# Kernel tuning notes

Measured on AMD Instinct MI355X. Metric: run time of the kernel, lower is better.

Reference implementation:

```python
import jax, jax.numpy as jnp
import numpy as np

N = 50000      # number of atoms/nodes
D = 32         # atom_dim == units (pad_length = 0)
E = 300000     # number of bonds/edges
BD = 16        # bond_dim
STEPS = 4      # message passing steps


def setup_inputs() -> dict:
    key = jax.random.key(0)
    ks = jax.random.split(key, 8)
    atom_features = jax.random.normal(ks[0], (N, D), dtype=jnp.float32)
    bond_features = jax.random.uniform(ks[1], (E, BD), dtype=jnp.float32)
    pair_indices = jax.random.randint(ks[2], (E, 2), 0, N, dtype=jnp.int32)
    # EdgeNetwork kernel: xavier_uniform on [bond_dim, atom_dim*atom_dim]
    s = float(np.sqrt(6.0 / (BD + D * D)))
    kernel = jax.random.uniform(ks[3], (BD, D * D), dtype=jnp.float32, minval=-s, maxval=s)
    bias = jnp.zeros((D * D,), dtype=jnp.float32)
    # torch.nn.GRUCell init: U(-1/sqrt(H), 1/sqrt(H)), H = D (pad_length = 0)
    stdv = float(1.0 / np.sqrt(D))
    W_ih = jax.random.uniform(ks[4], (3 * D, D), dtype=jnp.float32, minval=-stdv, maxval=stdv)
    W_hh = jax.random.uniform(ks[5], (3 * D, D), dtype=jnp.float32, minval=-stdv, maxval=stdv)
    b_ih = jax.random.uniform(ks[6], (3 * D,), dtype=jnp.float32, minval=-stdv, maxval=stdv)
    b_hh = jax.random.uniform(ks[7], (3 * D,), dtype=jnp.float32, minval=-stdv, maxval=stdv)
    return {
        "atom_features": atom_features,
        "bond_features": bond_features,
        "pair_indices": pair_indices,
        "kernel": kernel,
        "bias": bias,
        "W_ih": W_ih,
        "W_hh": W_hh,
        "b_ih": b_ih,
        "b_hh": b_hh,
    }


def _gru_cell(x, h, W_ih, W_hh, b_ih, b_hh):
    # torch.nn.GRUCell math, gates stacked as (r, z, n)
    gi = x @ W_ih.T + b_ih  # [N, 3D]
    gh = h @ W_hh.T + b_hh  # [N, 3D]
    i_r, i_z, i_n = jnp.split(gi, 3, axis=-1)
    h_r, h_z, h_n = jnp.split(gh, 3, axis=-1)
    r = jax.nn.sigmoid(i_r + h_r)
    z = jax.nn.sigmoid(i_z + h_z)
    n = jnp.tanh(i_n + r * h_n)
    return (1.0 - z) * n + z * h


def reference(atom_features, bond_features, pair_indices, kernel, bias, W_ih, W_hh, b_ih, b_hh):
    # pad_length = units - atom_dim = 0, so no padding needed.
    W = kernel.reshape(BD, D, D)   # per-bond-feature DxD transforms
    Bm = bias.reshape(D, D)        # bias as DxD matrix applied to neighbor feats
    dst = pair_indices[:, 0]       # aggregation (index_add) target
    src = pair_indices[:, 1]       # gathered neighbor

    h = atom_features
    for _ in range(STEPS):
        nbr = h[src]  # [E, D] gather
        # transformed[e, i] = sum_j (bond[e] @ kernel + bias)[i, j] * nbr[e, j]
        msg = jnp.einsum('eb,bij,ej->ei', bond_features, W, nbr) + nbr @ Bm.T
        agg = jax.ops.segment_sum(msg, dst, num_segments=N)  # scatter-add
        h = _gru_cell(agg, h, W_ih, W_hh, b_ih, b_hh)
    return h
```

## Files before the change

kernel.cpp:

```cpp
#include <hip/hip_runtime.h>
#include <math.h>

#define N_ATOMS 50000
#define D 32
#define E_EDGES 300000
#define BD 16
#define SW 544
#define PADN 50176
#define SCAN_BLOCKS 196
#define GRU_TILE 8
#define GRU_NT (N_ATOMS / GRU_TILE)

#define NB 16
#define FBLOCKS ((N_ATOMS + NB - 1) / NB)

__device__ __forceinline__ float sigmoidf_(float x) {
    return 1.0f / (1.0f + __expf(-x));
}


__global__ void k_build_wt(const float* __restrict__ kern,
                           const float* __restrict__ bias,
                           float* __restrict__ WTj) {
    int idx = blockIdx.x * 256 + threadIdx.x;
    if (idx >= 32 * SW) return;
    int j = idx / SW;
    int r = idx - j * SW;
    int b = r >> 5, i = r & 31;
    WTj[idx] = (b < BD) ? kern[b * 1024 + i * 32 + j] : bias[i * 32 + j];
}

__global__ void k_hist(const int* __restrict__ pair, int* __restrict__ deg) {
    int e = blockIdx.x * 256 + threadIdx.x;
    if (e < E_EDGES) atomicAdd(&deg[pair[2 * e + 1]], 1);
}

__global__ void k_scan1(const int* __restrict__ deg, int* __restrict__ offs,
                        int* __restrict__ bsums) {
    __shared__ int sm[256];
    int t = threadIdx.x, gid = blockIdx.x * 256 + t;
    int v = deg[gid];
    sm[t] = v;
    __syncthreads();
    for (int off = 1; off < 256; off <<= 1) {
        int x = (t >= off) ? sm[t - off] : 0;
        __syncthreads();
        sm[t] += x;
        __syncthreads();
    }
    offs[gid] = sm[t] - v;
    if (t == 255) bsums[blockIdx.x] = sm[255];
}

__global__ void k_scan2(const int* __restrict__ bsums, int* __restrict__ boffs, int nb) {
    __shared__ int sm[256];
    int t = threadIdx.x;
    int v = (t < nb) ? bsums[t] : 0;
    sm[t] = v;
    __syncthreads();
    for (int off = 1; off < 256; off <<= 1) {
        int x = (t >= off) ? sm[t - off] : 0;
        __syncthreads();
        sm[t] += x;
        __syncthreads();
    }
    if (t < nb) boffs[t] = sm[t] - v;
}

__global__ void k_scan3(int* __restrict__ offs, const int* __restrict__ boffs) {
    int gid = blockIdx.x * 256 + threadIdx.x;
    offs[gid] += boffs[blockIdx.x];
}

__global__ void k_scatter_perm(const int* __restrict__ pair, const int* __restrict__ offs,
                               int* __restrict__ cursor, const float* __restrict__ bond,
                               float* __restrict__ bond_perm, int* __restrict__ dstid) {
    int e = blockIdx.x * 256 + threadIdx.x;
    if (e >= E_EDGES) return;
    int d = pair[2 * e], s = pair[2 * e + 1];
    int pos = offs[s] + atomicAdd(&cursor[s], 1);
    dstid[pos] = d;
    const float4* src4 = (const float4*)(bond + (size_t)e * BD);
    float4* dst4 = (float4*)(bond_perm + (size_t)pos * BD);
    dst4[0] = src4[0];
    dst4[1] = src4[1];
    dst4[2] = src4[2];
    dst4[3] = src4[3];
}

#define EDGE_FMA(M, B0, B1, B2, B3, YN) do {            \
    M = fmaf(B0.x, YN[0],  M); M = fmaf(B0.y, YN[1],  M); \
    M = fmaf(B0.z, YN[2],  M); M = fmaf(B0.w, YN[3],  M); \
    M = fmaf(B1.x, YN[4],  M); M = fmaf(B1.y, YN[5],  M); \
    M = fmaf(B1.z, YN[6],  M); M = fmaf(B1.w, YN[7],  M); \
    M = fmaf(B2.x, YN[8],  M); M = fmaf(B2.y, YN[9],  M); \
    M = fmaf(B2.z, YN[10], M); M = fmaf(B2.w, YN[11], M); \
    M = fmaf(B3.x, YN[12], M); M = fmaf(B3.y, YN[13], M); \
    M = fmaf(B3.z, YN[14], M); M = fmaf(B3.w, YN[15], M); \
} while (0)

__global__ __launch_bounds__(256, 4)
void k_fused(const float* __restrict__ h_in, float* __restrict__ agg,
             const float* __restrict__ bond_perm, const int* __restrict__ dstid,
             const float* __restrict__ WTj,
             const int* __restrict__ offs, const int* __restrict__ deg) {
    __shared__ float h_lds[NB][33];

    const int t = threadIdx.x;
    const int bbase = blockIdx.x * NB;
    const int i = t & 31;
    const int grp = t >> 5;
    const int hn0 = grp * 2;

    {
        const int n = t >> 5;
        h_lds[n][i]     = h_in[(size_t)(bbase + n) * D + i];
        h_lds[n + 8][i] = h_in[(size_t)(bbase + n + 8) * D + i];
    }

    int stv[2], env[2];
#pragma unroll
    for (int n = 0; n < 2; ++n) {
        const int node = bbase + hn0 + n;
        const int o = offs[node];
        stv[n] = o;
        env[n] = o + deg[node];
    }
    __syncthreads();

    float y[2][17];
#pragma unroll
    for (int n = 0; n < 2; ++n)
#pragma unroll
        for (int b = 0; b < 17; ++b) y[n][b] = 0.f;

    for (int j = 0; j < 32; ++j) {
        float wv[17];
#pragma unroll
        for (int b = 0; b < 17; ++b)
            wv[b] = WTj[j * SW + b * 32 + i];
        const float hv0 = h_lds[hn0][j];
        const float hv1 = h_lds[hn0 + 1][j];
#pragma unroll
        for (int b = 0; b < 17; ++b) {
            y[0][b] = fmaf(wv[b], hv0, y[0][b]);
            y[1][b] = fmaf(wv[b], hv1, y[1][b]);
        }
    }

#pragma unroll
    for (int n = 0; n < 2; ++n) {
        int p = stv[n];
        const int e = env[n];
        for (; p + 2 <= e; p += 2) {
            const float4* bp0 = (const float4*)(bond_perm + (size_t)p * BD);
            const float4* bp1 = (const float4*)(bond_perm + (size_t)(p + 1) * BD);
            const int d0 = dstid[p];
            const int d1 = dstid[p + 1];
            const float4 a0 = bp0[0], a1 = bp0[1], a2 = bp0[2], a3 = bp0[3];
            const float4 c0 = bp1[0], c1 = bp1[1], c2 = bp1[2], c3 = bp1[3];
            float m0 = y[n][16];
            float m1 = y[n][16];
            EDGE_FMA(m0, a0, a1, a2, a3, y[n]);
            EDGE_FMA(m1, c0, c1, c2, c3, y[n]);
            atomicAdd(&agg[(size_t)d0 * D + i], m0);
            atomicAdd(&agg[(size_t)d1 * D + i], m1);
        }
        if (p < e) {
            const float4* bp0 = (const float4*)(bond_perm + (size_t)p * BD);
            const int d0 = dstid[p];
            const float4 a0 = bp0[0], a1 = bp0[1], a2 = bp0[2], a3 = bp0[3];
            float m0 = y[n][16];
            EDGE_FMA(m0, a0, a1, a2, a3, y[n]);
            atomicAdd(&agg[(size_t)d0 * D + i], m0);
        }
    }
}

__global__ __launch_bounds__(256, 2)
void k_gru(float* __restrict__ agg_g, const float* __restrict__ h_in,
           float* __restrict__ h_out,
           const float* __restrict__ Wih, const float* __restrict__ Whh,
           const float* __restrict__ bih, const float* __restrict__ bhh) {
    __shared__ float Wih_s[96][33];
    __shared__ float Whh_s[96][33];
    __shared__ float bih_s[96], bhh_s[96];
    __shared__ float x_lds[GRU_TILE][32];
    __shared__ float h_lds[GRU_TILE][32];

    const int t = threadIdx.x;

    for (int idx = t; idx < 96 * 32; idx += 256) {
        const int o = idx >> 5, jj = idx & 31;
        Wih_s[o][jj] = Wih[idx];
        Whh_s[o][jj] = Whh[idx];
    }
    if (t < 96) { bih_s[t] = bih[t]; bhh_s[t] = bhh[t]; }

    const int r = t >> 5;
    const int i = t & 31;
    const int stride = gridDim.x;

    int tile = blockIdx.x;
    float xr = 0.f, hr = 0.f;
    if (tile < GRU_NT) {
        xr = agg_g[tile * 256 + t];
        hr = h_in[tile * 256 + t];
    }
    for (; tile < GRU_NT; tile += stride) {
        ((float*)x_lds)[t] = xr;
        ((float*)h_lds)[t] = hr;
        agg_g[tile * 256 + t] = 0.f;
        __syncthreads();
        const int nxt = tile + stride;
        if (nxt < GRU_NT) {
            xr = agg_g[nxt * 256 + t];
            hr = h_in[nxt * 256 + t];
        }
        float gri = bih_s[i],      grh = bhh_s[i];
        float gzi = bih_s[32 + i], gzh = bhh_s[32 + i];
        float gni = bih_s[64 + i], gnh = bhh_s[64 + i];
#pragma unroll 8
        for (int jj = 0; jj < 32; ++jj) {
            const float xv = x_lds[r][jj];
            const float hv = h_lds[r][jj];
            gri = fmaf(Wih_s[i][jj],      xv, gri);
            gzi = fmaf(Wih_s[32 + i][jj], xv, gzi);
            gni = fmaf(Wih_s[64 + i][jj], xv, gni);
            grh = fmaf(Whh_s[i][jj],      hv, grh);
            gzh = fmaf(Whh_s[32 + i][jj], hv, gzh);
            gnh = fmaf(Whh_s[64 + i][jj], hv, gnh);
        }
        const float rg = sigmoidf_(gri + grh);
        const float zg = sigmoidf_(gzi + gzh);
        float xn = gni + rg * gnh;
        xn = fminf(fmaxf(xn, -15.f), 15.f);
        const float e2 = __expf(2.f * xn);
        const float ng = (e2 - 1.f) / (e2 + 1.f);
        h_out[tile * 256 + t] = (1.f - zg) * ng + zg * h_lds[r][i];
        __syncthreads();
    }
}

extern "C" void kernel_launch(void* const* d_in, const int* in_sizes, int n_in,
                              void* d_out, int out_size, void* d_ws, size_t ws_size,
                              hipStream_t stream) {
    const float* atom = (const float*)d_in[0];
    const float* bond = (const float*)d_in[1];
    const int*   pair = (const int*)d_in[2];
    const float* kern = (const float*)d_in[3];
    const float* bias = (const float*)d_in[4];
    const float* Wih  = (const float*)d_in[5];
    const float* Whh  = (const float*)d_in[6];
    const float* bih  = (const float*)d_in[7];
    const float* bhh  = (const float*)d_in[8];
    float* out = (float*)d_out;

    char* w = (char*)d_ws;
    auto alloc = [&](size_t bytes) {
        char* p = w;
        w += (bytes + 255) & ~size_t(255);
        return p;
    };
    float* hA        = (float*)alloc((size_t)N_ATOMS * D * 4);
    float* aggG      = (float*)alloc((size_t)N_ATOMS * D * 4);
    float* WTj       = (float*)alloc((size_t)32 * SW * 4);
    int*   degcur    = (int*)alloc((size_t)2 * PADN * 4);
    int*   offs      = (int*)alloc((size_t)PADN * 4);
    int*   bsums     = (int*)alloc(256 * 4);
    int*   boffs     = (int*)alloc(256 * 4);
    int*   dstid     = (int*)alloc((size_t)E_EDGES * 4);
    float* bond_perm = (float*)alloc((size_t)E_EDGES * BD * 4);
    int* deg    = degcur;
    int* cursor = degcur + PADN;

    hipMemsetAsync(degcur, 0, (size_t)2 * PADN * 4, stream);
    hipMemsetAsync(aggG, 0, (size_t)N_ATOMS * D * 4, stream);

    k_build_wt<<<(32 * SW + 255) / 256, 256, 0, stream>>>(kern, bias, WTj);
    k_hist<<<(E_EDGES + 255) / 256, 256, 0, stream>>>(pair, deg);
    k_scan1<<<SCAN_BLOCKS, 256, 0, stream>>>(deg, offs, bsums);
    k_scan2<<<1, 256, 0, stream>>>(bsums, boffs, SCAN_BLOCKS);
    k_scan3<<<SCAN_BLOCKS, 256, 0, stream>>>(offs, boffs);
    k_scatter_perm<<<(E_EDGES + 255) / 256, 256, 0, stream>>>(pair, offs, cursor,
                                                              bond, bond_perm, dstid);

    const float* hsrc = atom;
    float* hdst[4] = { hA, out, hA, out };
    for (int s = 0; s < 4; ++s) {
        k_fused<<<FBLOCKS, 256, 0, stream>>>(hsrc, aggG, bond_perm, dstid,
                                             WTj, offs, deg);
        k_gru<<<2048, 256, 0, stream>>>(aggG, hsrc, hdst[s], Wih, Whh, bih, bhh);
        hsrc = hdst[s];
    }
}
```

Before: 526.1 us.

## Process four nodes per warp in fused edge kernel with double-buffered weight loads

Doubles the node tile per block (16 to 32) so each 32-lane group computes the per-node 17x32 projections for four nodes, reusing each loaded weight column across more nodes. Weight column loads are double-buffered across j iterations to overlap global loads with FMAs, and bounds checks are added for the partial last block. Launch bounds drop to 2 blocks per CU to allow the larger register footprint (y[4][17] plus two weight buffers), and the GRU grid is halved. The trade-off is lower occupancy and fewer blocks, which may hurt latency hiding in the atomic-heavy edge loop.

```diff
diff --git a/kernel.cpp b/kernel.cpp
--- a/kernel.cpp
+++ b/kernel.cpp
@@ -11,7 +11,7 @@
 #define GRU_TILE 8
 #define GRU_NT (N_ATOMS / GRU_TILE)
 
-#define NB 16
+#define NB 32
 #define FBLOCKS ((N_ATOMS + NB - 1) / NB)
 
 __device__ __forceinline__ float sigmoidf_(float x) {
@@ -99,7 +99,23 @@
     M = fmaf(B3.z, YN[14], M); M = fmaf(B3.w, YN[15], M); \
 } while (0)
 
-__global__ __launch_bounds__(256, 4)
+#define LOAD_WV(WVA, JJ) do {                           \
+    _Pragma("unroll")                                   \
+    for (int b = 0; b < 17; ++b)                        \
+        WVA[b] = WTj[(JJ) * SW + b * 32 + i];           \
+} while (0)
+
+#define FMA_WV(WVA, JJ) do {                            \
+    _Pragma("unroll")                                   \
+    for (int n = 0; n < 4; ++n) {                       \
+        const float hv = h_lds[hn0 + n][(JJ)];          \
+        _Pragma("unroll")                               \
+        for (int b = 0; b < 17; ++b)                    \
+            y[n][b] = fmaf(WVA[b], hv, y[n][b]);        \
+    }                                                   \
+} while (0)
+
+__global__ __launch_bounds__(256, 2)
 void k_fused(const float* __restrict__ h_in, float* __restrict__ agg,
              const float* __restrict__ bond_perm, const int* __restrict__ dstid,
              const float* __restrict__ WTj,
@@ -110,46 +126,46 @@
     const int bbase = blockIdx.x * NB;
     const int i = t & 31;
     const int grp = t >> 5;
-    const int hn0 = grp * 2;
+    const int hn0 = grp * 4;
+
+#pragma unroll
+    for (int k = 0; k < 4; ++k) {
+        const int idx = t + 256 * k;
+        const int n = idx >> 5, j = idx & 31;
+        const int node = bbase + n;
+        h_lds[n][j] = (node < N_ATOMS) ? h_in[(size_t)node * D + j] : 0.f;
+    }
+
+    int stv[4], env[4];
+#pragma unroll
+    for (int n = 0; n < 4; ++n) {
+        const int node = bbase + hn0 + n;
+        const bool ok = (node < N_ATOMS);
+        const int o = ok ? offs[node] : 0;
+        stv[n] = o;
+        env[n] = o + (ok ? deg[node] : 0);
+    }
+    __syncthreads();
+
+    float y[4][17];
+#pragma unroll
+    for (int n = 0; n < 4; ++n)
+#pragma unroll
+        for (int b = 0; b < 17; ++b) y[n][b] = 0.f;
 
     {
-        const int n = t >> 5;
-        h_lds[n][i]     = h_in[(size_t)(bbase + n) * D + i];
-        h_lds[n + 8][i] = h_in[(size_t)(bbase + n + 8) * D + i];
-    }
-
-    int stv[2], env[2];
-#pragma unroll
-    for (int n = 0; n < 2; ++n) {
-        const int node = bbase + hn0 + n;
-        const int o = offs[node];
-        stv[n] = o;
-        env[n] = o + deg[node];
-    }
-    __syncthreads();
-
-    float y[2][17];
-#pragma unroll
-    for (int n = 0; n < 2; ++n)
-#pragma unroll
-        for (int b = 0; b < 17; ++b) y[n][b] = 0.f;
-
-    for (int j = 0; j < 32; ++j) {
-        float wv[17];
-#pragma unroll
-        for (int b = 0; b < 17; ++b)
-            wv[b] = WTj[j * SW + b * 32 + i];
-        const float hv0 = h_lds[hn0][j];
-        const float hv1 = h_lds[hn0 + 1][j];
-#pragma unroll
-        for (int b = 0; b < 17; ++b) {
-            y[0][b] = fmaf(wv[b], hv0, y[0][b]);
-            y[1][b] = fmaf(wv[b], hv1, y[1][b]);
-        }
-    }
-
-#pragma unroll
-    for (int n = 0; n < 2; ++n) {
+        float wvA[17], wvB[17];
+        LOAD_WV(wvA, 0);
+        for (int j = 0; j < 32; j += 2) {
+            LOAD_WV(wvB, j + 1);
+            FMA_WV(wvA, j);
+            if (j + 2 < 32) LOAD_WV(wvA, j + 2);
+            FMA_WV(wvB, j + 1);
+        }
+    }
+
+#pragma unroll
+    for (int n = 0; n < 4; ++n) {
         int p = stv[n];
         const int e = env[n];
         for (; p + 2 <= e; p += 2) {
@@ -290,7 +306,7 @@
     for (int s = 0; s < 4; ++s) {
         k_fused<<<FBLOCKS, 256, 0, stream>>>(hsrc, aggG, bond_perm, dstid,
                                              WTj, offs, deg);
-        k_gru<<<2048, 256, 0, stream>>>(aggG, hsrc, hdst[s], Wih, Whh, bih, bhh);
+        k_gru<<<1024, 256, 0, stream>>>(aggG, hsrc, hdst[s], Wih, Whh, bih, bhh);
         hsrc = hdst[s];
     }
 }
```

New measurement: 480.4 us (median of 2 runs). 1.09x faster.
